# Optimization experiments

Hardware: AMD Instinct MI355X
Metric: run time of the kernel (lower is better)

Reference implementation:

```python
import jax, jax.numpy as jnp
import numpy as np
from jax import lax

B, H, W = 4096, 8, 8
DICT, SE, E, NZ = 64, 8, 256, 1024
C1, C2 = 64, 128
EPS = 1e-4


def setup_inputs() -> dict:
    key = jax.random.key(0)
    ks = jax.random.split(key, 32)
    d = {}
    d['s'] = jax.random.randint(ks[0], (B, H, W), 0, DICT)
    d['s_prime'] = jax.random.randint(ks[1], (B, H, W), 0, DICT)
    d['w_embed'] = jax.random.normal(ks[2], (DICT, SE), dtype=jnp.float32)
    i = 3
    for p in ('p1', 'p2', 'p3'):
        d[p + '_w1'] = jax.random.normal(ks[i], (C1, SE, 3, 3), dtype=jnp.float32) * 0.1; i += 1
        d[p + '_b1'] = jax.random.normal(ks[i], (C1,), dtype=jnp.float32) * 0.1; i += 1
        d[p + '_w2'] = jax.random.normal(ks[i], (C2, C1, 3, 3), dtype=jnp.float32) * 0.05; i += 1
        d[p + '_b2'] = jax.random.normal(ks[i], (C2,), dtype=jnp.float32) * 0.05; i += 1
        d[p + '_lw'] = jax.random.normal(ks[i], (E, C2 * H * W), dtype=jnp.float32) * 0.02; i += 1
        d[p + '_lb'] = jax.random.normal(ks[i], (E,), dtype=jnp.float32) * 0.02; i += 1
    d['z_vectors'] = jax.random.normal(ks[i], (NZ, E), dtype=jnp.float32)
    d['scale'] = jnp.ones((1,), dtype=jnp.float32)
    return d


def _conv(x, w, b):
    # x: [B,C,H,W], w: [O,I,3,3], padding=1 == SAME for k=3
    y = lax.conv_general_dilated(x, w, (1, 1), 'SAME',
                                 dimension_numbers=('NCHW', 'OIHW', 'NCHW'))
    return y + b[None, :, None, None]


def _phi(x, w1, b1, w2, b2, lw, lb):
    # run_modules(..., last_activation=True): relu after every conv
    x = jax.nn.relu(_conv(x, w1, b1))
    x = jax.nn.relu(_conv(x, w2, b2))
    x = x.reshape(x.shape[0], -1)  # [B, C2*H*W]
    return x @ lw.T + lb  # [B, E]


def _normalized(m, eps):
    return m / (jnp.sqrt(jnp.sum(m * m, axis=1, keepdims=True)) + eps)


def reference(s, s_prime, w_embed,
              p1_w1, p1_b1, p1_w2, p1_b2, p1_lw, p1_lb,
              p2_w1, p2_b1, p2_w2, p2_b2, p2_lw, p2_lb,
              p3_w1, p3_b1, p3_w2, p3_b2, p3_lw, p3_lb,
              z_vectors, scale):
    # nn.Embedding(max_norm=1): renorm rows with norm > 1 to unit norm
    wn = jnp.sqrt(jnp.sum(w_embed * w_embed, axis=1, keepdims=True))
    w = w_embed * jnp.minimum(1.0, 1.0 / jnp.maximum(wn, 1e-7))
    s_embed = jnp.transpose(w[s], (0, 3, 1, 2))        # [B,SE,H,W]
    sp_embed = jnp.transpose(w[s_prime], (0, 3, 1, 2))  # embed_conv is None -> identity

    s_int = _phi(s_embed, p1_w1, p1_b1, p1_w2, p1_b2, p1_lw, p1_lb)            # phi1
    diff_int = _phi(sp_embed - s_embed, p2_w1, p2_b1, p2_w2, p2_b2, p2_lw, p2_lb)  # phi2
    sp_out = _normalized(_phi(sp_embed, p3_w1, p3_b1, p3_w2, p3_b2, p3_lw, p3_lb), EPS)  # phi3

    # quantize: cdist (p=2) against codebook, argmax (farthest, as in source), gather
    x2 = jnp.sum(diff_int * diff_int, axis=1, keepdims=True)      # [B,1]
    z2 = jnp.sum(z_vectors * z_vectors, axis=1)[None, :]          # [1,NZ]
    dist = jnp.sqrt(jnp.maximum(x2 + z2 - 2.0 * (diff_int @ z_vectors.T), 0.0))  # [B,NZ]
    z_inds = jnp.argmax(dist, axis=1)                              # [B]
    z_matrix = z_vectors[z_inds]                                   # [B,E]

    s_out = _normalized(s_int + z_matrix, EPS)                     # fc (fc_sizes=None)
    gram = s_out @ sp_out.T                                        # [B,B]
    return jnp.exp(scale) * gram
```

## Files before the change

kernel.cpp:

```cpp
#include <hip/hip_runtime.h>
#include <hip/hip_bf16.h>
#include <math.h>

#define NB 4096
#define SE 8
#define ND 64
#define C1 64
#define C2 128
#define NE 256
#define NZ 1024
#define CHUNK 2048
#define KACT 8192
#define KSPLIT 16

#define W1M_N (3*64*96)
#define W2M_N (3*128*576)
#define ZT_N  (256*1024)
#define PREP_TOTAL (W1M_N + W2M_N + ZT_N)
#define LW_N (NE*KACT)

typedef __attribute__((ext_vector_type(8))) short bf16x8;
typedef __attribute__((ext_vector_type(4))) float f32x4;
typedef __attribute__((ext_vector_type(8))) unsigned short u16x8;
typedef __attribute__((ext_vector_type(4))) unsigned short u16x4;

static __device__ __forceinline__ unsigned short f2bf(float v) {
  __hip_bfloat16 h = __float2bfloat16(v);
  return __builtin_bit_cast(unsigned short, h);
}
static __device__ __forceinline__ float bf2f(unsigned short u) {
  return __bfloat162float(__builtin_bit_cast(__hip_bfloat16, u));
}

__global__ __launch_bounds__(256) void prep_kernel(
    const float* __restrict__ w1_0, const float* __restrict__ w1_1, const float* __restrict__ w1_2,
    const float* __restrict__ w2_0, const float* __restrict__ w2_1, const float* __restrict__ w2_2,
    const float* __restrict__ z,
    unsigned short* __restrict__ w1mh, unsigned short* __restrict__ w1ml,
    unsigned short* __restrict__ w2mh, unsigned short* __restrict__ w2ml,
    float* __restrict__ zT)
{
  int idx = blockIdx.x * 256 + threadIdx.x;
  if (idx < W1M_N) {
    int p = idx / 6144; int r = idx - p*6144; int o = r / 96; int q = r - o*96;
    int j = q >> 3; int c = q & 7;
    const float* w1 = (p == 0) ? w1_0 : (p == 1) ? w1_1 : w1_2;
    float v = (j < 9) ? w1[o*72 + c*9 + j] : 0.f;
    unsigned short h = f2bf(v);
    w1mh[idx] = h;
    w1ml[idx] = f2bf(v - bf2f(h));
  } else if (idx < W1M_N + W2M_N) {
    int r0 = idx - W1M_N;
    int p = r0 / (128*576); int r = r0 - p*(128*576);
    int o = r / 576; int rem = r - o*576; int j = rem >> 6; int c = rem & 63;
    const float* w2 = (p == 0) ? w2_0 : (p == 1) ? w2_1 : w2_2;
    float v = w2[o*576 + c*9 + j];
    unsigned short h = f2bf(v);
    w2mh[r0] = h;
    w2ml[r0] = f2bf(v - bf2f(h));
  } else if (idx < PREP_TOTAL) {
    int r = idx - (W1M_N + W2M_N);
    int e = r >> 10, n = r & 1023;
    zT[r] = z[n*256 + e];
  }
}

__global__ __launch_bounds__(256) void prep_lw_kernel(
    const float* __restrict__ lw, unsigned short* __restrict__ lwh,
    unsigned short* __restrict__ lwl, int do_lo)
{
  int idx = blockIdx.x * 256 + threadIdx.x;
  float v = lw[idx];
  unsigned short h = f2bf(v);
  lwh[idx] = h;
  if (do_lo) lwl[idx] = f2bf(v - bf2f(h));
}

template<int PASSES>
__global__ __launch_bounds__(256, 4) void conv_phi_kernel(
    const int* __restrict__ s, const int* __restrict__ sp,
    const float* __restrict__ w_embed,
    const unsigned short* __restrict__ w1mh, const unsigned short* __restrict__ w1ml,
    const float* __restrict__ b1,
    const unsigned short* __restrict__ w2mh, const unsigned short* __restrict__ w2ml,
    const float* __restrict__ b2,
    unsigned short* __restrict__ acth, unsigned short* __restrict__ actl,
    int mode, int b_start)
{
  __shared__ float wtab[ND][SE];
  __shared__ int sidx[64];
  __shared__ int spidx[64];
  __shared__ __align__(16) unsigned short xph[960];
  __shared__ __align__(16) unsigned short xpl[960];
  __shared__ __align__(16) unsigned short c1h[7680];
  __shared__ __align__(16) unsigned short c1l[7680];

  const int tid = threadIdx.x;
  const int b = b_start + blockIdx.x;

  {
    int4 z4 = {0,0,0,0};
    for (int t = tid; t < 120; t += 256) { ((int4*)xph)[t] = z4; ((int4*)xpl)[t] = z4; }
    for (int t = tid; t < 960; t += 256) { ((int4*)c1h)[t] = z4; ((int4*)c1l)[t] = z4; }
  }

  if (tid < 64) {
    sidx[tid] = s[b*64 + tid];
    float v[SE]; float ss = 0.f;
    #pragma unroll
    for (int c = 0; c < SE; ++c) { v[c] = w_embed[tid*SE + c]; ss += v[c]*v[c]; }
    float nrm = sqrtf(ss);
    float sc = fminf(1.f, 1.f / fmaxf(nrm, 1e-7f));
    #pragma unroll
    for (int c = 0; c < SE; ++c) wtab[tid][c] = v[c] * sc;
  } else if (tid < 128) {
    spidx[tid - 64] = sp[b*64 + tid - 64];
  }
  __syncthreads();

  if (tid < 64) {
    const int y = tid >> 3, x = tid & 7;
    const float* r0 = wtab[sidx[tid]];
    const float* r1 = wtab[spidx[tid]];
    u16x8 hv, lv;
    #pragma unroll
    for (int c = 0; c < SE; ++c) {
      float e0 = r0[c], e1 = r1[c];
      float v = (mode == 0) ? e0 : (mode == 1) ? (e1 - e0) : e1;
      unsigned short h = f2bf(v);
      hv[c] = h;
      lv[c] = f2bf(v - bf2f(h));
    }
    const int lin = (y + 1)*12 + (x + 1);
    *(u16x8*)(xph + lin*8) = hv;
    *(u16x8*)(xpl + lin*8) = lv;
  }
  __syncthreads();

  {
    const int lane = tid & 63, wid = tid >> 6;
    const int l15 = lane & 15, lk4 = lane >> 4;
    const int y0 = l15 >> 3, x0 = l15 & 7;
    const int o = (wid << 4) + l15;

    f32x4 a1[4];
    #pragma unroll
    for (int mf = 0; mf < 4; ++mf) a1[mf] = (f32x4){0.f,0.f,0.f,0.f};

    __builtin_amdgcn_s_setprio(1);
    #pragma unroll
    for (int kk = 0; kk < 3; ++kk) {
      const int j = (kk << 2) + lk4;
      const int jc = (j > 8) ? 8 : j;
      const int dy = jc / 3, dx = jc - 3*(jc/3);
      const bf16x8 Bh = *(const bf16x8*)(w1mh + o*96 + (kk << 5) + (lk4 << 3));
      const bf16x8 Bl = *(const bf16x8*)(w1ml + o*96 + (kk << 5) + (lk4 << 3));
      #pragma unroll
      for (int mf = 0; mf < 4; ++mf) {
        const int lin = ((mf << 1) + y0 + dy)*12 + x0 + dx;
        const bf16x8 Ah = *(const bf16x8*)(xph + (lin << 3));
        const bf16x8 Al = *(const bf16x8*)(xpl + (lin << 3));
        a1[mf] = __builtin_amdgcn_mfma_f32_16x16x32_bf16(Ah, Bh, a1[mf], 0, 0, 0);
        a1[mf] = __builtin_amdgcn_mfma_f32_16x16x32_bf16(Al, Bh, a1[mf], 0, 0, 0);
        a1[mf] = __builtin_amdgcn_mfma_f32_16x16x32_bf16(Ah, Bl, a1[mf], 0, 0, 0);
      }
    }
    __builtin_amdgcn_s_setprio(0);

    const float bb = b1[o];
    const int cb = o >> 3, o7 = o & 7;
    #pragma unroll
    for (int mf = 0; mf < 4; ++mf) {
      #pragma unroll
      for (int r2 = 0; r2 < 4; ++r2) {
        const int p = (mf << 4) + (lk4 << 2) + r2;
        const int y = p >> 3, x = p & 7;
        float v = fmaxf(a1[mf][r2] + bb, 0.f);
        unsigned short h = f2bf(v);
        const int lin = (y + 1)*12 + (x + 1);
        const int idx2 = (lin << 6) + ((cb ^ (lin & 7)) << 3) + o7;
        c1h[idx2] = h;
        c1l[idx2] = f2bf(v - bf2f(h));
      }
    }
  }
  __syncthreads();

  {
    const int lane = tid & 63, wid = tid >> 6;
    const int obase = wid << 5;
    const int l15 = lane & 15, lk4 = lane >> 4;
    const int y0b = l15 >> 3, x0 = l15 & 7;

    f32x4 acc[4][2];
    #pragma unroll
    for (int mf = 0; mf < 4; ++mf)
      #pragma unroll
      for (int nf = 0; nf < 2; ++nf) acc[mf][nf] = (f32x4){0.f,0.f,0.f,0.f};

    #pragma unroll
    for (int j = 0; j < 9; ++j) {
      const int dy = j / 3, dx = j - 3*(j/3);
      #pragma unroll
      for (int h2 = 0; h2 < 2; ++h2) {
        const int kofs = j*64 + h2*32 + lk4*8;
        bf16x8 Bh[2], Bl[2];
        #pragma unroll
        for (int nf = 0; nf < 2; ++nf) {
          const int orow = obase + nf*16 + l15;
          Bh[nf] = *(const bf16x8*)(w2mh + orow*576 + kofs);
          if (PASSES == 3) Bl[nf] = *(const bf16x8*)(w2ml + orow*576 + kofs);
        }
        const int cb = h2*4 + lk4;
        bf16x8 Ah[4], Al[4];
        #pragma unroll
        for (int mf = 0; mf < 4; ++mf) {
          const int yy = mf*2 + y0b + dy;
          const int xx = x0 + dx;
          const int lin = yy*12 + xx;
          const int idx2 = lin*64 + ((cb ^ (lin & 7)) << 3);
          Ah[mf] = *(const bf16x8*)(c1h + idx2);
          Al[mf] = *(const bf16x8*)(c1l + idx2);
        }
        __builtin_amdgcn_s_setprio(1);
        #pragma unroll
        for (int mf = 0; mf < 4; ++mf) {
          #pragma unroll
          for (int nf = 0; nf < 2; ++nf) {
            acc[mf][nf] = __builtin_amdgcn_mfma_f32_16x16x32_bf16(Ah[mf], Bh[nf], acc[mf][nf], 0, 0, 0);
            acc[mf][nf] = __builtin_amdgcn_mfma_f32_16x16x32_bf16(Al[mf], Bh[nf], acc[mf][nf], 0, 0, 0);
            if (PASSES == 3)
              acc[mf][nf] = __builtin_amdgcn_mfma_f32_16x16x32_bf16(Ah[mf], Bl[nf], acc[mf][nf], 0, 0, 0);
          }
        }
        __builtin_amdgcn_s_setprio(0);
      }
    }

    #pragma unroll
    for (int nf = 0; nf < 2; ++nf) {
      const int col = obase + nf*16 + l15;
      const float bv = b2[col];
      #pragma unroll
      for (int mf = 0; mf < 4; ++mf) {
        const int p0 = mf*16 + lk4*4;
        u16x4 hv, lv;
        #pragma unroll
        for (int r2 = 0; r2 < 4; ++r2) {
          float v = fmaxf(acc[mf][nf][r2] + bv, 0.f);
          unsigned short hq = f2bf(v);
          hv[r2] = hq;
          lv[r2] = f2bf(v - bf2f(hq));
        }
        *(u16x4*)(acth + (size_t)blockIdx.x*8192 + col*64 + p0) = hv;
        if (PASSES == 3)
          *(u16x4*)(actl + (size_t)blockIdx.x*8192 + col*64 + p0) = lv;
      }
    }
  }
}

template<int PASSES>
__global__ __launch_bounds__(256) void gemm_lds_tn(
    const unsigned short* __restrict__ Ahp, const unsigned short* __restrict__ Alp,
    const unsigned short* __restrict__ Bhp, const unsigned short* __restrict__ Blp,
    int K, float* __restrict__ Cdirect, float* __restrict__ Cpart,
    const float* __restrict__ bias, const float* __restrict__ scale_ptr)
{
  constexpr int NOP = (PASSES == 3) ? 2 : 1;
  __shared__ __align__(16) unsigned short As[NOP][128*64];
  __shared__ __align__(16) unsigned short Bs[NOP][64*64];

  const int tid = threadIdx.x;
  const int lane = tid & 63, wid = tid >> 6;
  const int wm = wid >> 1, wn = wid & 1;
  const int l15 = lane & 15, lk4 = lane >> 4;
  const int M = gridDim.x << 7, N = gridDim.y << 6;
  const int KC = K / gridDim.z;
  const int bm = blockIdx.x << 7, bn = blockIdx.y << 6;
  const int kbase = blockIdx.z * KC;
  const int NT = KC >> 6;

  const int sr = tid >> 3;
  const int sc8 = (tid & 7) * 8;

  const unsigned short* gA[NOP];
  const unsigned short* gB[NOP];
  gA[0] = Ahp; gB[0] = Bhp;
  if (PASSES == 3) { gA[1] = Alp; gB[1] = Blp; }

  u16x8 ra[NOP][4], rb[NOP][2];

  f32x4 acc[4][2];
  #pragma unroll
  for (int fm = 0; fm < 4; ++fm)
    #pragma unroll
    for (int nf = 0; nf < 2; ++nf) acc[fm][nf] = (f32x4){0.f,0.f,0.f,0.f};

  {
    const int k0 = kbase + sc8;
    #pragma unroll
    for (int p = 0; p < NOP; ++p) {
      #pragma unroll
      for (int i = 0; i < 4; ++i)
        ra[p][i] = *(const u16x8*)(gA[p] + (size_t)(bm + sr + i*32) * K + k0);
      #pragma unroll
      for (int i = 0; i < 2; ++i)
        rb[p][i] = *(const u16x8*)(gB[p] + (size_t)(bn + sr + i*32) * K + k0);
    }
  }

  for (int t = 0; t < NT; ++t) {
    __syncthreads();
    #pragma unroll
    for (int p = 0; p < NOP; ++p) {
      #pragma unroll
      for (int i = 0; i < 4; ++i) {
        const int r = sr + i*32;
        *(u16x8*)(&As[p][r*64 + (sc8 ^ ((r & 7) << 3))]) = ra[p][i];
      }
      #pragma unroll
      for (int i = 0; i < 2; ++i) {
        const int r = sr + i*32;
        *(u16x8*)(&Bs[p][r*64 + (sc8 ^ ((r & 7) << 3))]) = rb[p][i];
      }
    }
    __syncthreads();
    if (t + 1 < NT) {
      const int k0 = kbase + ((t + 1) << 6) + sc8;
      #pragma unroll
      for (int p = 0; p < NOP; ++p) {
        #pragma unroll
        for (int i = 0; i < 4; ++i)
          ra[p][i] = *(const u16x8*)(gA[p] + (size_t)(bm + sr + i*32) * K + k0);
        #pragma unroll
        for (int i = 0; i < 2; ++i)
          rb[p][i] = *(const u16x8*)(gB[p] + (size_t)(bn + sr + i*32) * K + k0);
      }
    }
    #pragma unroll
    for (int ks = 0; ks < 2; ++ks) {
      const int kb = ks*32 + lk4*8;
      bf16x8 af[NOP][4], bf[NOP][2];
      #pragma unroll
      for (int p = 0; p < NOP; ++p) {
        #pragma unroll
        for (int fm = 0; fm < 4; ++fm) {
          const int r = wm*64 + fm*16 + l15;
          af[p][fm] = *(const bf16x8*)(&As[p][r*64 + (kb ^ ((r & 7) << 3))]);
        }
        #pragma unroll
        for (int nf = 0; nf < 2; ++nf) {
          const int r = wn*32 + nf*16 + l15;
          bf[p][nf] = *(const bf16x8*)(&Bs[p][r*64 + (kb ^ ((r & 7) << 3))]);
        }
      }
      #pragma unroll
      for (int fm = 0; fm < 4; ++fm) {
        #pragma unroll
        for (int nf = 0; nf < 2; ++nf) {
          acc[fm][nf] = __builtin_amdgcn_mfma_f32_16x16x32_bf16(af[0][fm], bf[0][nf], acc[fm][nf], 0, 0, 0);
          if (PASSES == 3) {
            acc[fm][nf] = __builtin_amdgcn_mfma_f32_16x16x32_bf16(af[0][fm], bf[1][nf], acc[fm][nf], 0, 0, 0);
            acc[fm][nf] = __builtin_amdgcn_mfma_f32_16x16x32_bf16(af[1][fm], bf[0][nf], acc[fm][nf], 0, 0, 0);
          }
        }
      }
    }
  }

  if (Cpart) {
    float* base = Cpart + (size_t)blockIdx.z * ((size_t)M * N);
    #pragma unroll
    for (int fm = 0; fm < 4; ++fm) {
      #pragma unroll
      for (int nf = 0; nf < 2; ++nf) {
        const int row0 = bm + wm*64 + fm*16 + lk4*4;
        const int col  = bn + wn*32 + nf*16 + l15;
        #pragma unroll
        for (int r2 = 0; r2 < 4; ++r2)
          base[(size_t)(row0 + r2) * N + col] = acc[fm][nf][r2];
      }
    }
  } else {
    float alpha = scale_ptr ? expf(scale_ptr[0]) : 1.f;
    #pragma unroll
    for (int fm = 0; fm < 4; ++fm) {
      #pragma unroll
      for (int nf = 0; nf < 2; ++nf) {
        const int row0 = bm + wm*64 + fm*16 + lk4*4;
        const int col  = bn + wn*32 + nf*16 + l15;
        const float bv = bias ? bias[col] : 0.f;
        #pragma unroll
        for (int r2 = 0; r2 < 4; ++r2)
          Cdirect[(size_t)(row0 + r2) * N + col] = alpha * acc[fm][nf][r2] + bv;
      }
    }
  }
}

__global__ __launch_bounds__(256) void reduce_bias_kernel(
    const float* __restrict__ part, const float* __restrict__ bias, float* __restrict__ out)
{
  const int idx = blockIdx.x * 256 + threadIdx.x;
  float a = bias[idx & (NE-1)];
  #pragma unroll
  for (int q = 0; q < KSPLIT; ++q) a += part[(size_t)q * (CHUNK*NE) + idx];
  out[idx] = a;
}

__global__ __launch_bounds__(256) void quant_kernel(
    const float* __restrict__ diff, const float* __restrict__ zT, int* __restrict__ z_ind)
{
  __shared__ __align__(16) float d[8][NE];
  __shared__ float wv[8][4];
  __shared__ int wni[8][4];
  const int tid = threadIdx.x;
  const int b0 = blockIdx.x * 8;
  for (int j = tid; j < 8*NE; j += 256) (&d[0][0])[j] = diff[(size_t)b0*NE + j];
  __syncthreads();

  float zz[4] = {0.f, 0.f, 0.f, 0.f};
  float dot[8][4] = {};
  for (int e = 0; e < NE; e += 4) {
    float4 dd[8];
    #pragma unroll
    for (int r = 0; r < 8; ++r) dd[r] = *(const float4*)(&d[r][e]);
    #pragma unroll
    for (int u = 0; u < 4; ++u) {
      const float* zr = zT + (size_t)(e + u) * NZ + tid;
      float z0 = zr[0], z1 = zr[256], z2 = zr[512], z3 = zr[768];
      zz[0] = fmaf(z0, z0, zz[0]); zz[1] = fmaf(z1, z1, zz[1]);
      zz[2] = fmaf(z2, z2, zz[2]); zz[3] = fmaf(z3, z3, zz[3]);
      #pragma unroll
      for (int r = 0; r < 8; ++r) {
        const float de = (u == 0) ? dd[r].x : (u == 1) ? dd[r].y : (u == 2) ? dd[r].z : dd[r].w;
        dot[r][0] = fmaf(z0, de, dot[r][0]);
        dot[r][1] = fmaf(z1, de, dot[r][1]);
        dot[r][2] = fmaf(z2, de, dot[r][2]);
        dot[r][3] = fmaf(z3, de, dot[r][3]);
      }
    }
  }

  const int lane = tid & 63, wid = tid >> 6;
  #pragma unroll
  for (int r = 0; r < 8; ++r) {
    float best = zz[0] - 2.f*dot[r][0]; int bi = tid;
    float v1 = zz[1] - 2.f*dot[r][1]; if (v1 > best) { best = v1; bi = tid + 256; }
    float v2 = zz[2] - 2.f*dot[r][2]; if (v2 > best) { best = v2; bi = tid + 512; }
    float v3 = zz[3] - 2.f*dot[r][3]; if (v3 > best) { best = v3; bi = tid + 768; }
    for (int m = 1; m < 64; m <<= 1) {
      float ov = __shfl_xor(best, m, 64);
      int   oi = __shfl_xor(bi, m, 64);
      if (ov > best || (ov == best && oi < bi)) { best = ov; bi = oi; }
    }
    if (lane == 0) { wv[r][wid] = best; wni[r][wid] = bi; }
  }
  __syncthreads();
  if (tid < 8) {
    float best = wv[tid][0]; int bi = wni[tid][0];
    #pragma unroll
    for (int w = 1; w < 4; ++w) {
      float v = wv[tid][w]; int n = wni[tid][w];
      if (v > best || (v == best && n < bi)) { best = v; bi = n; }
    }
    z_ind[b0 + tid] = bi;
  }
}

__global__ __launch_bounds__(256) void norm_to_bf16_kernel(
    const float* __restrict__ v, unsigned short* __restrict__ ob)
{
  const int row = blockIdx.x*4 + (threadIdx.x >> 6);
  const int lane = threadIdx.x & 63;
  float4 x = ((const float4*)v)[(size_t)row*64 + lane];
  float ss = x.x*x.x + x.y*x.y + x.z*x.z + x.w*x.w;
  #pragma unroll
  for (int m = 1; m < 64; m <<= 1) ss += __shfl_xor(ss, m, 64);
  float sc = 1.f / (sqrtf(ss) + 1e-4f);
  u16x4 o;
  o[0] = f2bf(x.x*sc); o[1] = f2bf(x.y*sc); o[2] = f2bf(x.z*sc); o[3] = f2bf(x.w*sc);
  *(u16x4*)(ob + (size_t)row*NE + lane*4) = o;
}

__global__ __launch_bounds__(256) void build_sout_kernel(
    const float* __restrict__ s_int, const float* __restrict__ z,
    const int* __restrict__ z_ind, unsigned short* __restrict__ ob)
{
  const int row = blockIdx.x*4 + (threadIdx.x >> 6);
  const int lane = threadIdx.x & 63;
  const int zi = z_ind[row];
  float4 a = *((const float4*)s_int + (size_t)row*64 + lane);
  float4 c = *((const float4*)z + (size_t)zi*64 + lane);
  float4 x = {a.x + c.x, a.y + c.y, a.z + c.z, a.w + c.w};
  float ss = x.x*x.x + x.y*x.y + x.z*x.z + x.w*x.w;
  #pragma unroll
  for (int m = 1; m < 64; m <<= 1) ss += __shfl_xor(ss, m, 64);
  float sc = 1.f / (sqrtf(ss) + 1e-4f);
  u16x4 o;
  o[0] = f2bf(x.x*sc); o[1] = f2bf(x.y*sc); o[2] = f2bf(x.z*sc); o[3] = f2bf(x.w*sc);
  *(u16x4*)(ob + (size_t)row*NE + lane*4) = o;
}

extern "C" void kernel_launch(void* const* d_in, const int* in_sizes, int n_in,
                              void* d_out, int out_size, void* d_ws, size_t ws_size,
                              hipStream_t stream)
{
  const int* s  = (const int*)d_in[0];
  const int* sp = (const int*)d_in[1];
  const float* w_embed = (const float*)d_in[2];
  const float* z = (const float*)d_in[21];
  const float* scale = (const float*)d_in[22];
  float* out = (float*)d_out;

  size_t off = 0;
  auto allocB = [&](size_t bytes) -> void* {
    void* p = (void*)((char*)d_ws + off);
    off += ((bytes + 255) & ~(size_t)255);
    return p;
  };
  unsigned short* w1mh  = (unsigned short*)allocB((size_t)W1M_N * 2);
  unsigned short* w1ml  = (unsigned short*)allocB((size_t)W1M_N * 2);
  unsigned short* w2mh  = (unsigned short*)allocB((size_t)W2M_N * 2);
  unsigned short* w2ml  = (unsigned short*)allocB((size_t)W2M_N * 2);
  float* zT             = (float*)allocB(ZT_N * 4);
  unsigned short* lwh   = (unsigned short*)allocB((size_t)LW_N * 2);
  unsigned short* lwl   = (unsigned short*)allocB((size_t)LW_N * 2);
  float* s_int          = (float*)allocB((size_t)NB * NE * 4);
  float* diff_int       = (float*)allocB((size_t)NB * NE * 4);
  float* sp_out         = (float*)allocB((size_t)NB * NE * 4);
  unsigned short* soutb = (unsigned short*)allocB((size_t)NB * NE * 2);
  unsigned short* spoutb= (unsigned short*)allocB((size_t)NB * NE * 2);
  int*   z_ind          = (int*)allocB(NB * 4);
  float* part           = (float*)allocB((size_t)CHUNK * NE * KSPLIT * 4);

  unsigned short* acth = (unsigned short*)d_out;
  unsigned short* actl = acth + (size_t)CHUNK * KACT;

  prep_kernel<<<PREP_TOTAL/256, 256, 0, stream>>>(
      (const float*)d_in[3],  (const float*)d_in[9],  (const float*)d_in[15],
      (const float*)d_in[5],  (const float*)d_in[11], (const float*)d_in[17],
      z, w1mh, w1ml, w2mh, w2ml, zT);

  for (int phi = 0; phi < 3; ++phi) {
    const float* b1 = (const float*)d_in[4 + phi*6];
    const float* b2 = (const float*)d_in[6 + phi*6];
    const float* lw = (const float*)d_in[7 + phi*6];
    const float* lb = (const float*)d_in[8 + phi*6];
    float* outvec = (phi == 0) ? s_int : (phi == 1) ? diff_int : sp_out;

    prep_lw_kernel<<<LW_N/256, 256, 0, stream>>>(lw, lwh, lwl, phi == 1);

    for (int b0 = 0; b0 < NB; b0 += CHUNK) {
      if (phi == 1)
        conv_phi_kernel<3><<<CHUNK, 256, 0, stream>>>(
            s, sp, w_embed, w1mh + phi*6144, w1ml + phi*6144, b1,
            w2mh + phi*(128*576), w2ml + phi*(128*576), b2,
            acth, actl, phi, b0);
      else
        conv_phi_kernel<2><<<CHUNK, 256, 0, stream>>>(
            s, sp, w_embed, w1mh + phi*6144, w1ml + phi*6144, b1,
            w2mh + phi*(128*576), w2ml + phi*(128*576), b2,
            acth, actl, phi, b0);
      dim3 g(CHUNK/128, NE/64, KSPLIT);
      if (phi == 1)
        gemm_lds_tn<3><<<g, 256, 0, stream>>>(acth, actl, lwh, lwl,
            KACT, nullptr, part, nullptr, nullptr);
      else
        gemm_lds_tn<1><<<g, 256, 0, stream>>>(acth, nullptr, lwh, nullptr,
            KACT, nullptr, part, nullptr, nullptr);
      reduce_bias_kernel<<<(CHUNK*NE)/256, 256, 0, stream>>>(part, lb, outvec + (size_t)b0*NE);
    }
  }

  norm_to_bf16_kernel<<<NB/4, 256, 0, stream>>>(sp_out, spoutb);
  quant_kernel<<<NB/8, 256, 0, stream>>>(diff_int, zT, z_ind);
  build_sout_kernel<<<NB/4, 256, 0, stream>>>(s_int, z, z_ind, soutb);

  dim3 gg(NB/128, NB/64, 1);
  gemm_lds_tn<1><<<gg, 256, 0, stream>>>(soutb, nullptr, spoutb, nullptr,
      NE, out, nullptr, nullptr, scale);
}
```

Before: 647.1 us.

## Process two images per conv block with wider per-wave output tiles; halve K-split

The conv kernel now handles two batch images per block. Two waves share each image, and each wave computes 64 output channels in conv2 (acc 4x4) instead of 32, so each A fragment loaded from LDS feeds more MFMAs. Conv1 is restructured so weights act as the M operand, with vectorized bias and packed stores. Launch bounds drop to 2 blocks per CU to allow more registers, and the linear GEMM K-split is halved from 16 to 8 to cut partial-sum traffic, at the cost of less occupancy and parallelism.

```diff
diff --git a/kernel.cpp b/kernel.cpp
--- a/kernel.cpp
+++ b/kernel.cpp
@@ -11,7 +11,7 @@
 #define NZ 1024
 #define CHUNK 2048
 #define KACT 8192
-#define KSPLIT 16
+#define KSPLIT 8
 
 #define W1M_N (3*64*96)
 #define W2M_N (3*128*576)
@@ -77,7 +77,7 @@
 }
 
 template<int PASSES>
-__global__ __launch_bounds__(256, 4) void conv_phi_kernel(
+__global__ __launch_bounds__(256, 2) void conv_phi_kernel(
     const int* __restrict__ s, const int* __restrict__ sp,
     const float* __restrict__ w_embed,
     const unsigned short* __restrict__ w1mh, const unsigned short* __restrict__ w1ml,
@@ -88,24 +88,25 @@
     int mode, int b_start)
 {
   __shared__ float wtab[ND][SE];
-  __shared__ int sidx[64];
-  __shared__ int spidx[64];
-  __shared__ __align__(16) unsigned short xph[960];
-  __shared__ __align__(16) unsigned short xpl[960];
-  __shared__ __align__(16) unsigned short c1h[7680];
-  __shared__ __align__(16) unsigned short c1l[7680];
+  __shared__ int sidx[128];
+  __shared__ int spidx[128];
+  __shared__ __align__(16) unsigned short xph[2][960];
+  __shared__ __align__(16) unsigned short xpl[2][960];
+  __shared__ __align__(16) unsigned short c1h[2][7680];
+  __shared__ __align__(16) unsigned short c1l[2][7680];
 
   const int tid = threadIdx.x;
-  const int b = b_start + blockIdx.x;
+  const int b0 = b_start + blockIdx.x * 2;
 
   {
     int4 z4 = {0,0,0,0};
-    for (int t = tid; t < 120; t += 256) { ((int4*)xph)[t] = z4; ((int4*)xpl)[t] = z4; }
-    for (int t = tid; t < 960; t += 256) { ((int4*)c1h)[t] = z4; ((int4*)c1l)[t] = z4; }
-  }
-
+    for (int t = tid; t < 240; t += 256) { ((int4*)xph)[t] = z4; ((int4*)xpl)[t] = z4; }
+    for (int t = tid; t < 1920; t += 256) { ((int4*)c1h)[t] = z4; ((int4*)c1l)[t] = z4; }
+  }
+
+  if (tid < 128) sidx[tid] = s[b0*64 + tid];
+  else spidx[tid - 128] = sp[b0*64 + tid - 128];
   if (tid < 64) {
-    sidx[tid] = s[b*64 + tid];
     float v[SE]; float ss = 0.f;
     #pragma unroll
     for (int c = 0; c < SE; ++c) { v[c] = w_embed[tid*SE + c]; ss += v[c]*v[c]; }
@@ -113,13 +114,13 @@
     float sc = fminf(1.f, 1.f / fmaxf(nrm, 1e-7f));
     #pragma unroll
     for (int c = 0; c < SE; ++c) wtab[tid][c] = v[c] * sc;
-  } else if (tid < 128) {
-    spidx[tid - 64] = sp[b*64 + tid - 64];
   }
   __syncthreads();
 
-  if (tid < 64) {
-    const int y = tid >> 3, x = tid & 7;
+  if (tid < 128) {
+    const int im = tid >> 6;
+    const int p = tid & 63;
+    const int y = p >> 3, x = p & 7;
     const float* r0 = wtab[sidx[tid]];
     const float* r1 = wtab[spidx[tid]];
     u16x8 hv, lv;
@@ -132,55 +133,74 @@
       lv[c] = f2bf(v - bf2f(h));
     }
     const int lin = (y + 1)*12 + (x + 1);
-    *(u16x8*)(xph + lin*8) = hv;
-    *(u16x8*)(xpl + lin*8) = lv;
+    *(u16x8*)(&xph[im][lin*8]) = hv;
+    *(u16x8*)(&xpl[im][lin*8]) = lv;
   }
   __syncthreads();
 
   {
     const int lane = tid & 63, wid = tid >> 6;
+    const int im = wid >> 1, ph = wid & 1;
     const int l15 = lane & 15, lk4 = lane >> 4;
-    const int y0 = l15 >> 3, x0 = l15 & 7;
-    const int o = (wid << 4) + l15;
-
-    f32x4 a1[4];
-    #pragma unroll
-    for (int mf = 0; mf < 4; ++mf) a1[mf] = (f32x4){0.f,0.f,0.f,0.f};
-
-    __builtin_amdgcn_s_setprio(1);
+
+    f32x4 a1[4][2];
+    #pragma unroll
+    for (int fm = 0; fm < 4; ++fm)
+      #pragma unroll
+      for (int nf = 0; nf < 2; ++nf) a1[fm][nf] = (f32x4){0.f,0.f,0.f,0.f};
+
     #pragma unroll
     for (int kk = 0; kk < 3; ++kk) {
       const int j = (kk << 2) + lk4;
       const int jc = (j > 8) ? 8 : j;
       const int dy = jc / 3, dx = jc - 3*(jc/3);
-      const bf16x8 Bh = *(const bf16x8*)(w1mh + o*96 + (kk << 5) + (lk4 << 3));
-      const bf16x8 Bl = *(const bf16x8*)(w1ml + o*96 + (kk << 5) + (lk4 << 3));
-      #pragma unroll
-      for (int mf = 0; mf < 4; ++mf) {
-        const int lin = ((mf << 1) + y0 + dy)*12 + x0 + dx;
-        const bf16x8 Ah = *(const bf16x8*)(xph + (lin << 3));
-        const bf16x8 Al = *(const bf16x8*)(xpl + (lin << 3));
-        a1[mf] = __builtin_amdgcn_mfma_f32_16x16x32_bf16(Ah, Bh, a1[mf], 0, 0, 0);
-        a1[mf] = __builtin_amdgcn_mfma_f32_16x16x32_bf16(Al, Bh, a1[mf], 0, 0, 0);
-        a1[mf] = __builtin_amdgcn_mfma_f32_16x16x32_bf16(Ah, Bl, a1[mf], 0, 0, 0);
-      }
-    }
-    __builtin_amdgcn_s_setprio(0);
-
-    const float bb = b1[o];
-    const int cb = o >> 3, o7 = o & 7;
-    #pragma unroll
-    for (int mf = 0; mf < 4; ++mf) {
-      #pragma unroll
-      for (int r2 = 0; r2 < 4; ++r2) {
-        const int p = (mf << 4) + (lk4 << 2) + r2;
-        const int y = p >> 3, x = p & 7;
-        float v = fmaxf(a1[mf][r2] + bb, 0.f);
-        unsigned short h = f2bf(v);
-        const int lin = (y + 1)*12 + (x + 1);
-        const int idx2 = (lin << 6) + ((cb ^ (lin & 7)) << 3) + o7;
-        c1h[idx2] = h;
-        c1l[idx2] = f2bf(v - bf2f(h));
+      bf16x8 Wh[4], Wl[4];
+      #pragma unroll
+      for (int fm = 0; fm < 4; ++fm) {
+        const int o = (fm << 4) + l15;
+        Wh[fm] = *(const bf16x8*)(w1mh + o*96 + (kk << 5) + (lk4 << 3));
+        Wl[fm] = *(const bf16x8*)(w1ml + o*96 + (kk << 5) + (lk4 << 3));
+      }
+      #pragma unroll
+      for (int nf = 0; nf < 2; ++nf) {
+        const int p = (ph << 5) + (nf << 4) + l15;
+        const int lin = ((p >> 3) + dy)*12 + (p & 7) + dx;
+        const bf16x8 Xh = *(const bf16x8*)(&xph[im][lin << 3]);
+        const bf16x8 Xl = *(const bf16x8*)(&xpl[im][lin << 3]);
+        __builtin_amdgcn_s_setprio(1);
+        #pragma unroll
+        for (int fm = 0; fm < 4; ++fm) {
+          a1[fm][nf] = __builtin_amdgcn_mfma_f32_16x16x32_bf16(Wh[fm], Xh, a1[fm][nf], 0, 0, 0);
+          a1[fm][nf] = __builtin_amdgcn_mfma_f32_16x16x32_bf16(Wl[fm], Xh, a1[fm][nf], 0, 0, 0);
+          a1[fm][nf] = __builtin_amdgcn_mfma_f32_16x16x32_bf16(Wh[fm], Xl, a1[fm][nf], 0, 0, 0);
+        }
+        __builtin_amdgcn_s_setprio(0);
+      }
+    }
+
+    #pragma unroll
+    for (int fm = 0; fm < 4; ++fm) {
+      const int obase = (fm << 4) + (lk4 << 2);
+      const float4 bv = *(const float4*)(b1 + obase);
+      const int cb = obase >> 3;
+      const int osub = obase & 7;
+      #pragma unroll
+      for (int nf = 0; nf < 2; ++nf) {
+        const int p = (ph << 5) + (nf << 4) + l15;
+        const int lin = ((p >> 3) + 1)*12 + (p & 7) + 1;
+        const int idx2 = (lin << 6) + ((cb ^ (lin & 7)) << 3) + osub;
+        u16x4 hv, lv;
+        {
+          float v0 = fmaxf(a1[fm][nf][0] + bv.x, 0.f);
+          float v1 = fmaxf(a1[fm][nf][1] + bv.y, 0.f);
+          float v2 = fmaxf(a1[fm][nf][2] + bv.z, 0.f);
+          float v3 = fmaxf(a1[fm][nf][3] + bv.w, 0.f);
+          hv[0] = f2bf(v0); hv[1] = f2bf(v1); hv[2] = f2bf(v2); hv[3] = f2bf(v3);
+          lv[0] = f2bf(v0 - bf2f(hv[0])); lv[1] = f2bf(v1 - bf2f(hv[1]));
+          lv[2] = f2bf(v2 - bf2f(hv[2])); lv[3] = f2bf(v3 - bf2f(hv[3]));
+        }
+        *(u16x4*)(&c1h[im][idx2]) = hv;
+        *(u16x4*)(&c1l[im][idx2]) = lv;
       }
     }
   }
@@ -188,15 +208,16 @@
 
   {
     const int lane = tid & 63, wid = tid >> 6;
-    const int obase = wid << 5;
+    const int im = wid >> 1;
+    const int ob = (wid & 1) << 6;
     const int l15 = lane & 15, lk4 = lane >> 4;
     const int y0b = l15 >> 3, x0 = l15 & 7;
 
-    f32x4 acc[4][2];
+    f32x4 acc[4][4];
     #pragma unroll
     for (int mf = 0; mf < 4; ++mf)
       #pragma unroll
-      for (int nf = 0; nf < 2; ++nf) acc[mf][nf] = (f32x4){0.f,0.f,0.f,0.f};
+      for (int nf = 0; nf < 4; ++nf) acc[mf][nf] = (f32x4){0.f,0.f,0.f,0.f};
 
     #pragma unroll
     for (int j = 0; j < 9; ++j) {
@@ -204,29 +225,27 @@
       #pragma unroll
       for (int h2 = 0; h2 < 2; ++h2) {
         const int kofs = j*64 + h2*32 + lk4*8;
-        bf16x8 Bh[2], Bl[2];
-        #pragma unroll
-        for (int nf = 0; nf < 2; ++nf) {
-          const int orow = obase + nf*16 + l15;
+        bf16x8 Bh[4], Bl[4];
+        #pragma unroll
+        for (int nf = 0; nf < 4; ++nf) {
+          const int orow = ob + (nf << 4) + l15;
           Bh[nf] = *(const bf16x8*)(w2mh + orow*576 + kofs);
           if (PASSES == 3) Bl[nf] = *(const bf16x8*)(w2ml + orow*576 + kofs);
         }
-        const int cb = h2*4 + lk4;
+        const int cbk = (h2 << 2) + lk4;
         bf16x8 Ah[4], Al[4];
         #pragma unroll
         for (int mf = 0; mf < 4; ++mf) {
-          const int yy = mf*2 + y0b + dy;
-          const int xx = x0 + dx;
-          const int lin = yy*12 + xx;
-          const int idx2 = lin*64 + ((cb ^ (lin & 7)) << 3);
-          Ah[mf] = *(const bf16x8*)(c1h + idx2);
-          Al[mf] = *(const bf16x8*)(c1l + idx2);
+          const int lin = ((mf << 1) + y0b + dy)*12 + x0 + dx;
+          const int idx2 = (lin << 6) + ((cbk ^ (lin & 7)) << 3);
+          Ah[mf] = *(const bf16x8*)(&c1h[im][idx2]);
+          Al[mf] = *(const bf16x8*)(&c1l[im][idx2]);
         }
         __builtin_amdgcn_s_setprio(1);
         #pragma unroll
         for (int mf = 0; mf < 4; ++mf) {
           #pragma unroll
-          for (int nf = 0; nf < 2; ++nf) {
+          for (int nf = 0; nf < 4; ++nf) {
             acc[mf][nf] = __builtin_amdgcn_mfma_f32_16x16x32_bf16(Ah[mf], Bh[nf], acc[mf][nf], 0, 0, 0);
             acc[mf][nf] = __builtin_amdgcn_mfma_f32_16x16x32_bf16(Al[mf], Bh[nf], acc[mf][nf], 0, 0, 0);
             if (PASSES == 3)
@@ -237,9 +256,10 @@
       }
     }
 
-    #pragma unroll
-    for (int nf = 0; nf < 2; ++nf) {
-      const int col = obase + nf*16 + l15;
+    const size_t rowbase = (size_t)(blockIdx.x*2 + im) * 8192;
+    #pragma unroll
+    for (int nf = 0; nf < 4; ++nf) {
+      const int col = ob + (nf << 4) + l15;
       const float bv = b2[col];
       #pragma unroll
       for (int mf = 0; mf < 4; ++mf) {
@@ -252,9 +272,9 @@
           hv[r2] = hq;
           lv[r2] = f2bf(v - bf2f(hq));
         }
-        *(u16x4*)(acth + (size_t)blockIdx.x*8192 + col*64 + p0) = hv;
+        *(u16x4*)(acth + rowbase + col*64 + p0) = hv;
         if (PASSES == 3)
-          *(u16x4*)(actl + (size_t)blockIdx.x*8192 + col*64 + p0) = lv;
+          *(u16x4*)(actl + rowbase + col*64 + p0) = lv;
       }
     }
   }
@@ -554,12 +574,12 @@
 
     for (int b0 = 0; b0 < NB; b0 += CHUNK) {
       if (phi == 1)
-        conv_phi_kernel<3><<<CHUNK, 256, 0, stream>>>(
+        conv_phi_kernel<3><<<CHUNK/2, 256, 0, stream>>>(
             s, sp, w_embed, w1mh + phi*6144, w1ml + phi*6144, b1,
             w2mh + phi*(128*576), w2ml + phi*(128*576), b2,
             acth, actl, phi, b0);
       else
-        conv_phi_kernel<2><<<CHUNK, 256, 0, stream>>>(
+        conv_phi_kernel<2><<<CHUNK/2, 256, 0, stream>>>(
             s, sp, w_embed, w1mh + phi*6144, w1ml + phi*6144, b1,
             w2mh + phi*(128*576), w2ml + phi*(128*576), b2,
             acth, actl, phi, b0);
```

Measured after the change: 641.8 us. About the same (-0.8%).

## Transpose conv1 MFMA operands for vectorized LDS stores and halve K-split

Applied to the files above, without the earlier changes.

The first conv's MFMA mapping is transposed so each wave owns 16 pixels and loops over four 16-channel fragments. Weights become the A operand and the pixel patch the B operand, which lets each lane hold four consecutive output channels. The ReLU/bias epilogue can then write packed 4x16-bit stores into the swizzled LDS buffer instead of scattered scalar stores, and bias loads become a float4. Separately, KSPLIT for the big linear GEMM is cut from 16 to 8, giving fewer partial-sum slices to reduce at the cost of less parallelism per output tile.

```diff
diff --git a/kernel.cpp b/kernel.cpp
--- a/kernel.cpp
+++ b/kernel.cpp
@@ -11,7 +11,7 @@
 #define NZ 1024
 #define CHUNK 2048
 #define KACT 8192
-#define KSPLIT 16
+#define KSPLIT 8
 
 #define W1M_N (3*64*96)
 #define W2M_N (3*128*576)
@@ -139,56 +139,67 @@
 
   {
     const int lane = tid & 63, wid = tid >> 6;
+    const int ph = wid;
     const int l15 = lane & 15, lk4 = lane >> 4;
-    const int y0 = l15 >> 3, x0 = l15 & 7;
-    const int o = (wid << 4) + l15;
 
     f32x4 a1[4];
     #pragma unroll
-    for (int mf = 0; mf < 4; ++mf) a1[mf] = (f32x4){0.f,0.f,0.f,0.f};
-
-    __builtin_amdgcn_s_setprio(1);
+    for (int fm = 0; fm < 4; ++fm) a1[fm] = (f32x4){0.f,0.f,0.f,0.f};
+
     #pragma unroll
     for (int kk = 0; kk < 3; ++kk) {
       const int j = (kk << 2) + lk4;
       const int jc = (j > 8) ? 8 : j;
       const int dy = jc / 3, dx = jc - 3*(jc/3);
-      const bf16x8 Bh = *(const bf16x8*)(w1mh + o*96 + (kk << 5) + (lk4 << 3));
-      const bf16x8 Bl = *(const bf16x8*)(w1ml + o*96 + (kk << 5) + (lk4 << 3));
-      #pragma unroll
-      for (int mf = 0; mf < 4; ++mf) {
-        const int lin = ((mf << 1) + y0 + dy)*12 + x0 + dx;
-        const bf16x8 Ah = *(const bf16x8*)(xph + (lin << 3));
-        const bf16x8 Al = *(const bf16x8*)(xpl + (lin << 3));
-        a1[mf] = __builtin_amdgcn_mfma_f32_16x16x32_bf16(Ah, Bh, a1[mf], 0, 0, 0);
-        a1[mf] = __builtin_amdgcn_mfma_f32_16x16x32_bf16(Al, Bh, a1[mf], 0, 0, 0);
-        a1[mf] = __builtin_amdgcn_mfma_f32_16x16x32_bf16(Ah, Bl, a1[mf], 0, 0, 0);
-      }
-    }
-    __builtin_amdgcn_s_setprio(0);
-
-    const float bb = b1[o];
-    const int cb = o >> 3, o7 = o & 7;
-    #pragma unroll
-    for (int mf = 0; mf < 4; ++mf) {
-      #pragma unroll
-      for (int r2 = 0; r2 < 4; ++r2) {
-        const int p = (mf << 4) + (lk4 << 2) + r2;
-        const int y = p >> 3, x = p & 7;
-        float v = fmaxf(a1[mf][r2] + bb, 0.f);
-        unsigned short h = f2bf(v);
-        const int lin = (y + 1)*12 + (x + 1);
-        const int idx2 = (lin << 6) + ((cb ^ (lin & 7)) << 3) + o7;
-        c1h[idx2] = h;
-        c1l[idx2] = f2bf(v - bf2f(h));
-      }
+      bf16x8 Wh[4], Wl[4];
+      #pragma unroll
+      for (int fm = 0; fm < 4; ++fm) {
+        const int o = (fm << 4) + l15;
+        Wh[fm] = *(const bf16x8*)(w1mh + o*96 + (kk << 5) + (lk4 << 3));
+        Wl[fm] = *(const bf16x8*)(w1ml + o*96 + (kk << 5) + (lk4 << 3));
+      }
+      const int p = (ph << 4) + l15;
+      const int lin = ((p >> 3) + dy)*12 + (p & 7) + dx;
+      const bf16x8 Xh = *(const bf16x8*)(xph + (lin << 3));
+      const bf16x8 Xl = *(const bf16x8*)(xpl + (lin << 3));
+      __builtin_amdgcn_s_setprio(1);
+      #pragma unroll
+      for (int fm = 0; fm < 4; ++fm) {
+        a1[fm] = __builtin_amdgcn_mfma_f32_16x16x32_bf16(Wh[fm], Xh, a1[fm], 0, 0, 0);
+        a1[fm] = __builtin_amdgcn_mfma_f32_16x16x32_bf16(Wl[fm], Xh, a1[fm], 0, 0, 0);
+        a1[fm] = __builtin_amdgcn_mfma_f32_16x16x32_bf16(Wh[fm], Xl, a1[fm], 0, 0, 0);
+      }
+      __builtin_amdgcn_s_setprio(0);
+    }
+
+    const int p = (ph << 4) + l15;
+    const int lin = ((p >> 3) + 1)*12 + (p & 7) + 1;
+    #pragma unroll
+    for (int fm = 0; fm < 4; ++fm) {
+      const int obase = (fm << 4) + (lk4 << 2);
+      const float4 bv = *(const float4*)(b1 + obase);
+      const int cb = obase >> 3;
+      const int osub = obase & 7;
+      const int idx2 = (lin << 6) + ((cb ^ (lin & 7)) << 3) + osub;
+      u16x4 hv, lv;
+      {
+        float v0 = fmaxf(a1[fm][0] + bv.x, 0.f);
+        float v1 = fmaxf(a1[fm][1] + bv.y, 0.f);
+        float v2 = fmaxf(a1[fm][2] + bv.z, 0.f);
+        float v3 = fmaxf(a1[fm][3] + bv.w, 0.f);
+        hv[0] = f2bf(v0); hv[1] = f2bf(v1); hv[2] = f2bf(v2); hv[3] = f2bf(v3);
+        lv[0] = f2bf(v0 - bf2f(hv[0])); lv[1] = f2bf(v1 - bf2f(hv[1]));
+        lv[2] = f2bf(v2 - bf2f(hv[2])); lv[3] = f2bf(v3 - bf2f(hv[3]));
+      }
+      *(u16x4*)(c1h + idx2) = hv;
+      *(u16x4*)(c1l + idx2) = lv;
     }
   }
   __syncthreads();
 
   {
     const int lane = tid & 63, wid = tid >> 6;
-    const int obase = wid << 5;
+    const int ob = wid << 5;
     const int l15 = lane & 15, lk4 = lane >> 4;
     const int y0b = l15 >> 3, x0 = l15 & 7;
 
@@ -207,18 +218,16 @@
         bf16x8 Bh[2], Bl[2];
         #pragma unroll
         for (int nf = 0; nf < 2; ++nf) {
-          const int orow = obase + nf*16 + l15;
+          const int orow = ob + (nf << 4) + l15;
           Bh[nf] = *(const bf16x8*)(w2mh + orow*576 + kofs);
           if (PASSES == 3) Bl[nf] = *(const bf16x8*)(w2ml + orow*576 + kofs);
         }
-        const int cb = h2*4 + lk4;
+        const int cbk = (h2 << 2) + lk4;
         bf16x8 Ah[4], Al[4];
         #pragma unroll
         for (int mf = 0; mf < 4; ++mf) {
-          const int yy = mf*2 + y0b + dy;
-          const int xx = x0 + dx;
-          const int lin = yy*12 + xx;
-          const int idx2 = lin*64 + ((cb ^ (lin & 7)) << 3);
+          const int lin = ((mf << 1) + y0b + dy)*12 + x0 + dx;
+          const int idx2 = (lin << 6) + ((cbk ^ (lin & 7)) << 3);
           Ah[mf] = *(const bf16x8*)(c1h + idx2);
           Al[mf] = *(const bf16x8*)(c1l + idx2);
         }
@@ -237,9 +246,10 @@
       }
     }
 
+    const size_t rowbase = (size_t)blockIdx.x * 8192;
     #pragma unroll
     for (int nf = 0; nf < 2; ++nf) {
-      const int col = obase + nf*16 + l15;
+      const int col = ob + (nf << 4) + l15;
       const float bv = b2[col];
       #pragma unroll
       for (int mf = 0; mf < 4; ++mf) {
@@ -252,9 +262,9 @@
           hv[r2] = hq;
           lv[r2] = f2bf(v - bf2f(hq));
         }
-        *(u16x4*)(acth + (size_t)blockIdx.x*8192 + col*64 + p0) = hv;
+        *(u16x4*)(acth + rowbase + col*64 + p0) = hv;
         if (PASSES == 3)
-          *(u16x4*)(actl + (size_t)blockIdx.x*8192 + col*64 + p0) = lv;
+          *(u16x4*)(actl + rowbase + col*64 + p0) = lv;
       }
     }
   }
```

Measured after the change: 656.0 us. No clear change (+1.4%).
